# Optimization experiments

Hardware: AMD Instinct MI355X
Metric: run time of the kernel (lower is better)

## Reference

```python
import jax, jax.numpy as jnp
import numpy as np

DIM = 128
D = 2 * DIM           # d_model = dim_hidden * 2
HEADS = 8
DEPTH = 2
DFF = 2048            # PyTorch TransformerEncoderLayer default dim_feedforward
N_NODES = 8192
NO_HOPS = 512
MAX_HOP_LEN = 16
N_LEVELS = 16
MAX_LEV_LEN = NO_HOPS // N_LEVELS  # 32, balanced levels
N_MASKED = 512
N_ENC = 13            # hop tfs 0..3, lev tfs 4..7, graph tfs 8..11, mcm 12 (0,4,8 unused = masked modality)


def setup_inputs() -> dict:
    key = jax.random.key(0)
    ks = jax.random.split(key, 16)
    s = 0.02
    return {
        "tokens": jax.random.normal(ks[0], (4, N_NODES, D), jnp.float32),
        "masked_tokens": jax.random.normal(ks[1], (N_MASKED, D), jnp.float32),
        "hop_nodes": jax.random.normal(ks[2], (1, D), jnp.float32),
        "level_nodes": jax.random.normal(ks[3], (1, D), jnp.float32),
        "graph_nodes": jax.random.normal(ks[4], (1, D), jnp.float32),
        "in_w": jax.random.normal(ks[5], (N_ENC, DEPTH, 3 * D, D), jnp.float32) * s,
        "in_b": jnp.zeros((N_ENC, DEPTH, 3 * D), jnp.float32),
        "out_w": jax.random.normal(ks[6], (N_ENC, DEPTH, D, D), jnp.float32) * s,
        "out_b": jnp.zeros((N_ENC, DEPTH, D), jnp.float32),
        "ff1_w": jax.random.normal(ks[7], (N_ENC, DEPTH, DFF, D), jnp.float32) * s,
        "ff1_b": jnp.zeros((N_ENC, DEPTH, DFF), jnp.float32),
        "ff2_w": jax.random.normal(ks[8], (N_ENC, DEPTH, D, DFF), jnp.float32) * s,
        "ff2_b": jnp.zeros((N_ENC, DEPTH, D), jnp.float32),
        "ln1_w": jnp.ones((N_ENC, DEPTH, D), jnp.float32),
        "ln1_b": jnp.zeros((N_ENC, DEPTH, D), jnp.float32),
        "ln2_w": jnp.ones((N_ENC, DEPTH, D), jnp.float32),
        "ln2_b": jnp.zeros((N_ENC, DEPTH, D), jnp.float32),
        "hop_list": jax.random.randint(ks[9], (3, NO_HOPS, MAX_HOP_LEN), 0, N_NODES),
        "hop_lev": jnp.tile(jnp.arange(NO_HOPS, dtype=jnp.int32) % N_LEVELS, (3, 1)),
        "hop_length": jax.random.randint(ks[10], (3, NO_HOPS), 1, MAX_HOP_LEN + 1),
    }


def _ln(x, w, b):
    mu = jnp.mean(x, axis=-1, keepdims=True)
    var = jnp.mean((x - mu) ** 2, axis=-1, keepdims=True)
    return (x - mu) / jnp.sqrt(var + 1e-5) * w + b


def _layer(x, kpm, p):
    # p: (in_w,in_b,out_w,out_b,ff1_w,ff1_b,ff2_w,ff2_b,ln1_w,ln1_b,ln2_w,ln2_b)
    in_w, in_b, out_w, out_b, f1w, f1b, f2w, f2b, l1w, l1b, l2w, l2b = p
    B, S, Dm = x.shape
    dh = Dm // HEADS
    qkv = x @ in_w.T + in_b                       # [B,S,3D]
    q, k, v = jnp.split(qkv, 3, axis=-1)
    q = q.reshape(B, S, HEADS, dh)
    k = k.reshape(B, S, HEADS, dh)
    v = v.reshape(B, S, HEADS, dh)
    sc = jnp.einsum('bqhd,bkhd->bhqk', q, k) / np.sqrt(dh).astype(np.float32)
    if kpm is not None:
        sc = jnp.where(kpm[:, None, None, :], -1e9, sc)
    a = jax.nn.softmax(sc, axis=-1)
    o = jnp.einsum('bhqk,bkhd->bqhd', a, v).reshape(B, S, Dm) @ out_w.T + out_b
    x = _ln(x + o, l1w, l1b)                      # post-norm (torch default)
    f = jax.nn.relu(x @ f1w.T + f1b) @ f2w.T + f2b
    return _ln(x + f, l2w, l2b)


def _encoder(x, kpm, params, eid):
    for l in range(DEPTH):
        x = _layer(x, kpm, tuple(P[eid, l] for P in params))
    return x


def reference(tokens, masked_tokens, hop_nodes, level_nodes, graph_nodes,
              in_w, in_b, out_w, out_b, ff1_w, ff1_b, ff2_w, ff2_b,
              ln1_w, ln1_b, ln2_w, ln2_b, hop_list, hop_lev, hop_length):
    params = (in_w, in_b, out_w, out_b, ff1_w, ff1_b, ff2_w, ff2_b,
              ln1_w, ln1_b, ln2_w, ln2_b)
    other = []
    for m in range(3):                 # non-masked modalities, modal_k = m+1
        mk = m + 1
        # --- hop transformer: CLS hop token + gathered node tokens per hop ---
        seq = tokens[mk][hop_list[m]]  # [NO_HOPS, L, D]
        seq = jnp.concatenate(
            [jnp.broadcast_to(hop_nodes[None], (NO_HOPS, 1, D)), seq], axis=1)
        kpm = jnp.arange(MAX_HOP_LEN + 1)[None, :] > hop_length[m][:, None]
        hop_tok = _encoder(seq, kpm, params, mk)[:, 0]            # [NO_HOPS, D]
        # --- group hops by level (pack, preserving hop order within level) ---
        lev = hop_lev[m]
        idx = jnp.arange(NO_HOPS)
        pos = jnp.sum((lev[None, :] == lev[:, None]) & (idx[None, :] < idx[:, None]), axis=-1)
        counts = jax.ops.segment_sum(jnp.ones(NO_HOPS, jnp.int32), lev, num_segments=N_LEVELS)
        grid = jnp.zeros((N_LEVELS, MAX_LEV_LEN, D), seq.dtype).at[lev, pos].set(hop_tok)
        grid = jnp.concatenate(
            [jnp.broadcast_to(level_nodes[None], (N_LEVELS, 1, D)), grid], axis=1)
        kpm2 = jnp.arange(MAX_LEV_LEN + 1)[None, :] > counts[:, None]
        lev_tok = _encoder(grid, kpm2, params, 4 + mk)[:, 0]      # [N_LEVELS, D]
        # --- graph transformer over CLS graph token + level tokens ---
        gseq = jnp.concatenate([graph_nodes, lev_tok], axis=0)[None]  # [1, N_LEVELS+1, D]
        g_tok = _encoder(gseq, None, params, 8 + mk)[:, 0]        # [1, D]
        other.append(jnp.concatenate([hop_tok, lev_tok, g_tok], axis=0))
    all_tok = jnp.concatenate([masked_tokens] + other, axis=0)[None]
    pred = _encoder(all_tok, None, params, 12)
    return pred[0, :N_MASKED]
```

## Files before the change

kernel.cpp:

```cpp
#include <hip/hip_runtime.h>

#define D_MODEL 256
#define HEADS 8
#define DH 32
#define DEPTH 2
#define DFF 2048
#define NO_HOPS 512
#define MAX_HOP_LEN 16
#define N_LEVELS 16
#define MAX_LEV_LEN 32
#define N_MASKED 512
#define N_NODES 8192
#define N_FINAL 2099
#define NLAY 26
#define NSPLIT 8

typedef float f32x4 __attribute__((ext_vector_type(4)));
typedef short bf16x8 __attribute__((ext_vector_type(8)));
typedef short short4v __attribute__((ext_vector_type(4)));

#define GLOAD_LDS16(gp, lp) __builtin_amdgcn_global_load_lds( \
    (const __attribute__((address_space(1))) unsigned int*)(gp), \
    (__attribute__((address_space(3))) unsigned int*)(lp), 16, 0, 0)

__device__ __forceinline__ unsigned short f2bf(float f)
{
    unsigned int u = __builtin_bit_cast(unsigned int, f);
    unsigned int r = u + 0x7FFFu + ((u >> 16) & 1u);
    return (unsigned short)(r >> 16);
}

__device__ __forceinline__ float bf2f(unsigned short u)
{
    unsigned int x = (unsigned int)u << 16;
    return __builtin_bit_cast(float, x);
}

__device__ __forceinline__ bf16x8 cvt8(float4 a, float4 b)
{
    bf16x8 r;
    r[0] = (short)f2bf(a.x); r[1] = (short)f2bf(a.y);
    r[2] = (short)f2bf(a.z); r[3] = (short)f2bf(a.w);
    r[4] = (short)f2bf(b.x); r[5] = (short)f2bf(b.y);
    r[6] = (short)f2bf(b.z); r[7] = (short)f2bf(b.w);
    return r;
}

__global__ void cvt_w(const float* __restrict__ src, unsigned short* __restrict__ dst, long n8)
{
    long i = (long)blockIdx.x * blockDim.x + threadIdx.x;
    if (i >= n8) return;
    const float4* s = reinterpret_cast<const float4*>(src) + i * 2;
    float4 a = s[0], b = s[1];
    *reinterpret_cast<bf16x8*>(dst + i * 8) = cvt8(a, b);
}

__global__ __launch_bounds__(256) void gemm_bb64(
    const unsigned short* __restrict__ A, const unsigned short* __restrict__ Wb,
    const float* __restrict__ bias, void* __restrict__ Yv,
    int M, int N, int K, int relu,
    unsigned long rsA, unsigned long xg, unsigned long wg, unsigned long bg, unsigned long yg)
{
    extern __shared__ unsigned short sh[];
    const int grp = blockIdx.z;
    const int t = threadIdx.x;
    const int lane = t & 63, wid = t >> 6;
    const int wr = wid >> 1, wc = wid & 1;
    const int rowbase = blockIdx.y * 64;
    const int colbase = blockIdx.x * 128;
    const unsigned short* Abase = A + (size_t)grp * xg;
    const unsigned short* Wbase = Wb + (size_t)grp * wg;

    const unsigned short* gA[2]; unsigned short* lA[2];
    const unsigned short* gB[4]; unsigned short* lB[4];
    #pragma unroll
    for (int j = 0; j < 2; ++j) {
        int c = j * 256 + t;
        int sr = c >> 3, p = c & 7;
        int lc = p ^ (sr & 7);
        int ar = rowbase + sr; if (ar >= M) ar = M - 1;
        gA[j] = Abase + (size_t)ar * rsA + lc * 8;
        lA[j] = sh + (j * 256 + (t & ~63)) * 8;
    }
    #pragma unroll
    for (int j = 0; j < 4; ++j) {
        int c = j * 256 + t;
        int sr = c >> 3, p = c & 7;
        int lc = p ^ (sr & 7);
        gB[j] = Wbase + (size_t)(colbase + sr) * K + lc * 8;
        lB[j] = sh + 8192 + (j * 256 + (t & ~63)) * 8;
    }

    f32x4 acc[2][4];
    #pragma unroll
    for (int m = 0; m < 2; ++m)
        #pragma unroll
        for (int n = 0; n < 4; ++n)
            acc[m][n] = (f32x4){0.f, 0.f, 0.f, 0.f};

    const int g = lane >> 4, rr = lane & 15;
    const int nt = K >> 6;

    #pragma unroll
    for (int j = 0; j < 2; ++j) GLOAD_LDS16(gA[j], lA[j]);
    #pragma unroll
    for (int j = 0; j < 4; ++j) GLOAD_LDS16(gB[j], lB[j]);

    int buf = 0;
    for (int tt = 0; tt < nt; ++tt) {
        if (tt + 1 < nt) {
            const int k1 = (tt + 1) << 6;
            const int oa = (buf ^ 1) * 4096;
            const int ob = (buf ^ 1) * 8192;
            #pragma unroll
            for (int j = 0; j < 2; ++j) GLOAD_LDS16(gA[j] + k1, lA[j] + oa);
            #pragma unroll
            for (int j = 0; j < 4; ++j) GLOAD_LDS16(gB[j] + k1, lB[j] + ob);
            asm volatile("s_waitcnt vmcnt(6)\n\ts_barrier" ::: "memory");
        } else {
            asm volatile("s_waitcnt vmcnt(0)\n\ts_barrier" ::: "memory");
        }
        const unsigned short* Ab = sh + buf * 4096;
        const unsigned short* Bb = sh + 8192 + buf * 8192;
        #pragma unroll
        for (int ks = 0; ks < 2; ++ks) {
            bf16x8 af[2], bfr[4];
            #pragma unroll
            for (int m = 0; m < 2; ++m) {
                int row = wr * 32 + m * 16 + rr;
                int lc = ks * 4 + g;
                af[m] = *reinterpret_cast<const bf16x8*>(&Ab[row * 64 + ((lc ^ (row & 7)) * 8)]);
            }
            #pragma unroll
            for (int n = 0; n < 4; ++n) {
                int col = wc * 64 + n * 16 + rr;
                int lc = ks * 4 + g;
                bfr[n] = *reinterpret_cast<const bf16x8*>(&Bb[col * 64 + ((lc ^ (col & 7)) * 8)]);
            }
            #pragma unroll
            for (int m = 0; m < 2; ++m)
                #pragma unroll
                for (int n = 0; n < 4; ++n)
                    acc[m][n] = __builtin_amdgcn_mfma_f32_16x16x32_bf16(af[m], bfr[n], acc[m][n], 0, 0, 0);
        }
        asm volatile("s_barrier" ::: "memory");
        buf ^= 1;
    }

    const int rg = lane >> 4;
    const float* bp = bias + (size_t)grp * bg;
    #pragma unroll
    for (int n = 0; n < 4; ++n) {
        int coll = wc * 64 + n * 16 + rr;
        float bv = bp[colbase + coll];
        #pragma unroll
        for (int m = 0; m < 2; ++m) {
            #pragma unroll
            for (int i = 0; i < 4; ++i) {
                int rowl = wr * 32 + m * 16 + rg * 4 + i;
                float v = acc[m][n][i] + bv;
                if (relu) v = fmaxf(v, 0.f);
                sh[rowl * 128 + coll] = f2bf(v);
            }
        }
    }
    __syncthreads();
    unsigned short* Y = (unsigned short*)Yv + (size_t)grp * yg;
    int row = t >> 2, seg = t & 3;
    int grow = rowbase + row;
    if (grow < M) {
        const unsigned short* s = &sh[row * 128 + seg * 32];
        unsigned short* d = Y + (size_t)grow * N + colbase + seg * 32;
        #pragma unroll
        for (int j = 0; j < 4; ++j)
            *reinterpret_cast<bf16x8*>(d + j * 8) = *reinterpret_cast<const bf16x8*>(s + j * 8);
    }
}

__global__ __launch_bounds__(256) void attn_small(
    const unsigned short* __restrict__ QKV, const int* __restrict__ lengths,
    unsigned short* __restrict__ O, int B, int S)
{
    __shared__ __align__(16) unsigned short Ksm[4][32][40];
    __shared__ __align__(16) unsigned short Vsm[4][32][40];
    __shared__ __align__(16) unsigned short Psm[4][32][40];
    const int t = threadIdx.x;
    const int w = t >> 6, lane = t & 63;
    const int l15 = lane & 15, g = lane >> 4;
    int bh = blockIdx.x * 4 + w;
    const int BH = B * HEADS;
    if (bh >= BH) bh = BH - 1;
    const int b = bh >> 3, h = bh & 7;
    const unsigned short* base = QKV + (size_t)b * S * (3 * D_MODEL);
    int len_eff = S - 1;
    if (lengths) { int L = lengths[b]; if (L < len_eff) len_eff = L; }

    {
        int key = lane >> 1, hf = lane & 1;
        int kg = key < S ? key : S - 1;
        const unsigned short* kp = base + (size_t)kg * (3 * D_MODEL) + D_MODEL + h * DH + hf * 16;
        bf16x8 k0 = *reinterpret_cast<const bf16x8*>(kp);
        bf16x8 k1 = *reinterpret_cast<const bf16x8*>(kp + 8);
        *reinterpret_cast<bf16x8*>(&Ksm[w][key][hf * 16]) = k0;
        *reinterpret_cast<bf16x8*>(&Ksm[w][key][hf * 16 + 8]) = k1;
        const unsigned short* vp = kp + D_MODEL;
        bf16x8 v0 = *reinterpret_cast<const bf16x8*>(vp);
        bf16x8 v1 = *reinterpret_cast<const bf16x8*>(vp + 8);
        #pragma unroll
        for (int i = 0; i < 8; ++i) {
            Vsm[w][hf * 16 + i][key]     = (unsigned short)v0[i];
            Vsm[w][hf * 16 + 8 + i][key] = (unsigned short)v1[i];
        }
    }
    bf16x8 qa[2];
    #pragma unroll
    for (int qf = 0; qf < 2; ++qf) {
        int q = qf * 16 + l15; if (q > S - 1) q = S - 1;
        qa[qf] = *reinterpret_cast<const bf16x8*>(base + (size_t)q * (3 * D_MODEL) + h * DH + g * 8);
    }
    __syncthreads();

    const float scale = 0.17677669529663687f;
    const f32x4 zero = (f32x4){0.f,0.f,0.f,0.f};
    f32x4 sc[2][2];
    #pragma unroll
    for (int kf = 0; kf < 2; ++kf) {
        bf16x8 kb = *reinterpret_cast<const bf16x8*>(&Ksm[w][kf * 16 + l15][g * 8]);
        #pragma unroll
        for (int qf = 0; qf < 2; ++qf)
            sc[qf][kf] = __builtin_amdgcn_mfma_f32_16x16x32_bf16(qa[qf], kb, zero, 0, 0, 0);
    }
    float rsum[2][4];
    #pragma unroll
    for (int qf = 0; qf < 2; ++qf) {
        #pragma unroll
        for (int kf = 0; kf < 2; ++kf) {
            if (kf * 16 + l15 > len_eff) sc[qf][kf] = (f32x4){-1e9f,-1e9f,-1e9f,-1e9f};
            else sc[qf][kf] *= scale;
        }
        #pragma unroll
        for (int r = 0; r < 4; ++r) {
            float mx = fmaxf(sc[qf][0][r], sc[qf][1][r]);
            mx = fmaxf(mx, __shfl_xor(mx, 1, 64));
            mx = fmaxf(mx, __shfl_xor(mx, 2, 64));
            mx = fmaxf(mx, __shfl_xor(mx, 4, 64));
            mx = fmaxf(mx, __shfl_xor(mx, 8, 64));
            float s0 = __expf(sc[qf][0][r] - mx);
            float s1 = __expf(sc[qf][1][r] - mx);
            sc[qf][0][r] = s0;
            sc[qf][1][r] = s1;
            float ss = s0 + s1;
            ss += __shfl_xor(ss, 1, 64);
            ss += __shfl_xor(ss, 2, 64);
            ss += __shfl_xor(ss, 4, 64);
            ss += __shfl_xor(ss, 8, 64);
            rsum[qf][r] = ss;
        }
    }
    #pragma unroll
    for (int qf = 0; qf < 2; ++qf)
        #pragma unroll
        for (int kf = 0; kf < 2; ++kf)
            #pragma unroll
            for (int r = 0; r < 4; ++r)
                Psm[w][qf * 16 + g * 4 + r][kf * 16 + l15] = f2bf(sc[qf][kf][r]);
    __syncthreads();

    f32x4 o[2][2];
    #pragma unroll
    for (int df = 0; df < 2; ++df) {
        bf16x8 vb = *reinterpret_cast<const bf16x8*>(&Vsm[w][df * 16 + l15][g * 8]);
        #pragma unroll
        for (int qf = 0; qf < 2; ++qf) {
            bf16x8 pa = *reinterpret_cast<const bf16x8*>(&Psm[w][qf * 16 + l15][g * 8]);
            o[qf][df] = __builtin_amdgcn_mfma_f32_16x16x32_bf16(pa, vb, zero, 0, 0, 0);
        }
    }
    #pragma unroll
    for (int qf = 0; qf < 2; ++qf)
        #pragma unroll
        for (int r = 0; r < 4; ++r) {
            int q = qf * 16 + g * 4 + r;
            if (q < S) {
                float inv = 1.f / rsum[qf][r];
                #pragma unroll
                for (int df = 0; df < 2; ++df)
                    O[((size_t)b * S + q) * D_MODEL + h * DH + df * 16 + l15] = f2bf(o[qf][df][r] * inv);
            }
        }
}

template<int SPLIT>
__global__ __launch_bounds__(256) void attn_flash(
    const unsigned short* __restrict__ QKV, const int* __restrict__ lengths,
    unsigned short* __restrict__ O, int B, int S,
    int NSv, float* __restrict__ pAcc, float* __restrict__ pMS)
{
    __shared__ __align__(16) unsigned short Kt[64][32];
    __shared__ __align__(16) unsigned short Vt[32][64];
    __shared__ __align__(16) unsigned short Pw[4][16][64];

    const int t = threadIdx.x;
    const int lane = t & 63, wid = t >> 6;
    const int l15 = lane & 15, g = lane >> 4;
    const int b = SPLIT ? 0 : blockIdx.z;
    const int sp = SPLIT ? blockIdx.z : 0;
    const int h = blockIdx.y;
    const int qb = blockIdx.x * 64 + wid * 16;
    const unsigned short* base = QKV + (size_t)b * S * (3 * D_MODEL);

    int len_eff = S - 1;
    if (lengths) { int L = lengths[b]; if (L < len_eff) len_eff = L; }

    const float scale = 0.17677669529663687f;
    int qrow = qb + l15; if (qrow > S - 1) qrow = S - 1;
    bf16x8 qa = *reinterpret_cast<const bf16x8*>(base + (size_t)qrow * (3 * D_MODEL) + h * DH + g * 8);

    float m[4], sum[4];
    f32x4 o[2];
    #pragma unroll
    for (int r = 0; r < 4; ++r) { m[r] = -3.0e38f; sum[r] = 0.f; }
    o[0] = (f32x4){0.f,0.f,0.f,0.f};
    o[1] = (f32x4){0.f,0.f,0.f,0.f};

    const int kl = t >> 2, cg = t & 3;
    const int ntiles_all = (S + 63) >> 6;
    int tstart = 0, tend = ntiles_all;
    if (SPLIT) {
        int chunkT = (ntiles_all + NSv - 1) / NSv;
        tstart = sp * chunkT;
        tend = tstart + chunkT;
        if (tend > ntiles_all) tend = ntiles_all;
    }

    for (int tt = tstart; tt < tend; ++tt) {
        const int kbase = tt * 64;
        {
            int key = kbase + kl; if (key > S - 1) key = S - 1;
            const unsigned short* kp = base + (size_t)key * (3 * D_MODEL) + D_MODEL + h * DH + cg * 8;
            *reinterpret_cast<bf16x8*>(&Kt[kl][cg * 8]) = *reinterpret_cast<const bf16x8*>(kp);
            bf16x8 vv = *reinterpret_cast<const bf16x8*>(kp + D_MODEL);
            #pragma unroll
            for (int i = 0; i < 8; ++i) {
                int d = cg * 8 + i;
                int c = ((kl >> 3) ^ (d & 7)) * 8 + (kl & 7);
                Vt[d][c] = (unsigned short)vv[i];
            }
        }
        __syncthreads();

        f32x4 sc[4];
        const f32x4 zero = (f32x4){0.f,0.f,0.f,0.f};
        #pragma unroll
        for (int f = 0; f < 4; ++f) {
            bf16x8 kf = *reinterpret_cast<const bf16x8*>(&Kt[f * 16 + l15][g * 8]);
            sc[f] = __builtin_amdgcn_mfma_f32_16x16x32_bf16(qa, kf, zero, 0, 0, 0);
            sc[f] *= scale;
        }
        #pragma unroll
        for (int f = 0; f < 4; ++f) {
            if (kbase + f * 16 + l15 > len_eff)
                sc[f] = (f32x4){-1e9f,-1e9f,-1e9f,-1e9f};
        }
        float cr[4];
        #pragma unroll
        for (int r = 0; r < 4; ++r) {
            float mx = fmaxf(fmaxf(sc[0][r], sc[1][r]), fmaxf(sc[2][r], sc[3][r]));
            mx = fmaxf(mx, __shfl_xor(mx, 1, 64));
            mx = fmaxf(mx, __shfl_xor(mx, 2, 64));
            mx = fmaxf(mx, __shfl_xor(mx, 4, 64));
            mx = fmaxf(mx, __shfl_xor(mx, 8, 64));
            float nm = fmaxf(m[r], mx);
            cr[r] = __expf(m[r] - nm);
            m[r] = nm;
            float ssum = 0.f;
            #pragma unroll
            for (int f = 0; f < 4; ++f) {
                float e = __expf(sc[f][r] - nm);
                sc[f][r] = e;
                ssum += e;
            }
            ssum += __shfl_xor(ssum, 1, 64);
            ssum += __shfl_xor(ssum, 2, 64);
            ssum += __shfl_xor(ssum, 4, 64);
            ssum += __shfl_xor(ssum, 8, 64);
            sum[r] = sum[r] * cr[r] + ssum;
            o[0][r] *= cr[r];
            o[1][r] *= cr[r];
        }
        #pragma unroll
        for (int f = 0; f < 4; ++f) {
            int chunk = f * 2 + (l15 >> 3);
            #pragma unroll
            for (int r = 0; r < 4; ++r) {
                int row = g * 4 + r;
                Pw[wid][row][(chunk ^ (row & 7)) * 8 + (l15 & 7)] = f2bf(sc[f][r]);
            }
        }
        #pragma unroll
        for (int s = 0; s < 2; ++s) {
            bf16x8 pa = *reinterpret_cast<const bf16x8*>(
                &Pw[wid][l15][((s * 4 + g) ^ (l15 & 7)) * 8]);
            #pragma unroll
            for (int jf = 0; jf < 2; ++jf) {
                int d = jf * 16 + l15;
                bf16x8 vb = *reinterpret_cast<const bf16x8*>(
                    &Vt[d][((s * 4 + g) ^ (d & 7)) * 8]);
                o[jf] = __builtin_amdgcn_mfma_f32_16x16x32_bf16(pa, vb, o[jf], 0, 0, 0);
            }
        }
        __syncthreads();
    }

    if (SPLIT) {
        #pragma unroll
        for (int r = 0; r < 4; ++r) {
            int qout = qb + g * 4 + r;
            if (qout < S) {
                size_t pb = ((size_t)qout * HEADS + h) * NSv + sp;
                pAcc[pb * 32 + l15]      = o[0][r];
                pAcc[pb * 32 + 16 + l15] = o[1][r];
                if (l15 == 0) { pMS[pb * 2] = m[r]; pMS[pb * 2 + 1] = sum[r]; }
            }
        }
    } else {
        #pragma unroll
        for (int r = 0; r < 4; ++r) {
            float inv = 1.f / sum[r];
            int qout = qb + g * 4 + r;
            if (qout < S) {
                #pragma unroll
                for (int jf = 0; jf < 2; ++jf)
                    O[((size_t)b * S + qout) * D_MODEL + h * DH + jf * 16 + l15] = f2bf(o[jf][r] * inv);
            }
        }
    }
}

__global__ void attn_merge(const float* __restrict__ pAcc, const float* __restrict__ pMS,
                           unsigned short* __restrict__ O, int S, int NS)
{
    int idx = blockIdx.x * blockDim.x + threadIdx.x;
    if (idx >= S * HEADS * DH) return;
    int d = idx & 31;
    int h = (idx >> 5) & 7;
    int q = idx >> 8;
    size_t base = ((size_t)q * HEADS + h) * NS;
    float mstar = -3.0e38f;
    for (int s = 0; s < NS; ++s) mstar = fmaxf(mstar, pMS[(base + s) * 2]);
    float ssum = 0.f, acc = 0.f;
    for (int s = 0; s < NS; ++s) {
        float mi = pMS[(base + s) * 2];
        float si = pMS[(base + s) * 2 + 1];
        float w = __expf(mi - mstar);
        ssum += si * w;
        acc += pAcc[(base + s) * 32 + d] * w;
    }
    O[(size_t)q * D_MODEL + h * DH + d] = f2bf(acc / ssum);
}

__global__ void add_ln_g(const unsigned short* __restrict__ Xin, const unsigned short* __restrict__ R,
                         const float* __restrict__ w, const float* __restrict__ b,
                         unsigned short* __restrict__ Xout,
                         int M, int rows_pg, unsigned long wg, unsigned long rsX)
{
    int row = blockIdx.x * 4 + (threadIdx.x >> 6);
    int lane = threadIdx.x & 63;
    if (row >= M) return;
    int g = row / rows_pg;
    const float* wp = w + (size_t)g * wg;
    const float* bp = b + (size_t)g * wg;
    short4v xv = *reinterpret_cast<const short4v*>(Xin + (size_t)row * rsX + lane * 4);
    short4v rv = *reinterpret_cast<const short4v*>(R + (size_t)row * D_MODEL + lane * 4);
    float v[4];
    float sum = 0.f;
    #pragma unroll
    for (int j = 0; j < 4; ++j) {
        v[j] = bf2f((unsigned short)xv[j]) + bf2f((unsigned short)rv[j]);
        sum += v[j];
    }
    #pragma unroll
    for (int o = 32; o > 0; o >>= 1) sum += __shfl_xor(sum, o, 64);
    float mu = sum * (1.f / D_MODEL);
    float sq = 0.f;
    #pragma unroll
    for (int j = 0; j < 4; ++j) { float dd = v[j] - mu; sq += dd * dd; }
    #pragma unroll
    for (int o = 32; o > 0; o >>= 1) sq += __shfl_xor(sq, o, 64);
    float inv = rsqrtf(sq * (1.f / D_MODEL) + 1e-5f);
    short4v xb;
    #pragma unroll
    for (int j = 0; j < 4; ++j) {
        float out = (v[j] - mu) * inv * wp[lane * 4 + j] + bp[lane * 4 + j];
        xb[j] = (short)f2bf(out);
    }
    *reinterpret_cast<short4v*>(Xout + (size_t)row * D_MODEL + lane * 4) = xb;
}

__global__ void build_hop_seq_g(const float* __restrict__ tok, const int* __restrict__ hlist,
                                const float* __restrict__ hop_nodes,
                                unsigned short* __restrict__ Xb, int nm)
{
    int idx = blockIdx.x * blockDim.x + threadIdx.x;
    const int per = NO_HOPS * (MAX_HOP_LEN + 1) * D_MODEL;
    if (idx >= nm * per) return;
    int g = idx / per, r = idx % per;
    int d = r & 255;
    int rest = r >> 8;
    int p = rest % (MAX_HOP_LEN + 1);
    int hh = rest / (MAX_HOP_LEN + 1);
    float v;
    if (p == 0) v = hop_nodes[d];
    else {
        int node = hlist[(size_t)g * NO_HOPS * MAX_HOP_LEN + hh * MAX_HOP_LEN + p - 1];
        v = tok[(size_t)g * N_NODES * D_MODEL + (size_t)node * D_MODEL + d];
    }
    Xb[idx] = f2bf(v);
}

__global__ void compute_pos_g(const int* __restrict__ hop_lev, int* __restrict__ pos,
                              int* __restrict__ counts)
{
    int g = blockIdx.x;
    const int* lev = hop_lev + (size_t)g * NO_HOPS;
    int i = threadIdx.x;
    int li = lev[i];
    int p = 0;
    for (int j = 0; j < i; ++j) p += (lev[j] == li);
    pos[(size_t)g * NO_HOPS + i] = p;
    if (i < N_LEVELS) {
        int c = 0;
        for (int j = 0; j < NO_HOPS; ++j) c += (lev[j] == i);
        counts[(size_t)g * N_LEVELS + i] = c;
    }
}

__global__ void build_level_init_g(const float* __restrict__ level_nodes,
                                   unsigned short* __restrict__ Gb, int nm)
{
    int idx = blockIdx.x * blockDim.x + threadIdx.x;
    const int per = N_LEVELS * (MAX_LEV_LEN + 1) * D_MODEL;
    if (idx >= nm * per) return;
    int r = idx % per;
    int d = r & 255;
    int p = (r >> 8) % (MAX_LEV_LEN + 1);
    float v = (p == 0) ? level_nodes[d] : 0.f;
    Gb[idx] = f2bf(v);
}

__global__ void scatter_hops_g(const float* __restrict__ hop_tok, const int* __restrict__ hop_lev,
                               const int* __restrict__ pos,
                               unsigned short* __restrict__ Gb, int nm)
{
    int idx = blockIdx.x * blockDim.x + threadIdx.x;
    const int per = NO_HOPS * D_MODEL;
    if (idx >= nm * per) return;
    int g = idx / per, r = idx % per;
    int d = r & 255;
    int i = r >> 8;
    int lv = hop_lev[(size_t)g * NO_HOPS + i];
    int ps = pos[(size_t)g * NO_HOPS + i];
    size_t dst = (size_t)g * N_LEVELS * (MAX_LEV_LEN + 1) * D_MODEL +
                 ((size_t)lv * (MAX_LEV_LEN + 1) + 1 + ps) * D_MODEL + d;
    Gb[dst] = f2bf(hop_tok[idx]);
}

__global__ void build_graph_seq_g(const float* __restrict__ graph_nodes,
                                  const float* __restrict__ lev_tok,
                                  unsigned short* __restrict__ Xb, int nm)
{
    int idx = blockIdx.x * blockDim.x + threadIdx.x;
    const int per = (N_LEVELS + 1) * D_MODEL;
    if (idx >= nm * per) return;
    int g = idx / per, r = idx % per;
    int d = r & 255;
    int p = r >> 8;
    float v = (p == 0) ? graph_nodes[d]
                       : lev_tok[(size_t)g * N_LEVELS * D_MODEL + (size_t)(p - 1) * D_MODEL + d];
    Xb[idx] = f2bf(v);
}

__global__ void build_final_seq(const float* __restrict__ masked, const float* __restrict__ hoptok,
                                const float* __restrict__ levtok, const float* __restrict__ gtok,
                                unsigned short* __restrict__ Xb)
{
    int idx = blockIdx.x * blockDim.x + threadIdx.x;
    const int total = N_FINAL * D_MODEL;
    if (idx >= total) return;
    int d = idx & 255;
    int r = idx >> 8;
    float v;
    if (r < N_MASKED) v = masked[idx];
    else {
        int t = r - N_MASKED;
        int m = t / 529;
        int w = t % 529;
        if (w < 512)      v = hoptok[((size_t)m * 512 + w) * D_MODEL + d];
        else if (w < 528) v = levtok[((size_t)m * 16 + (w - 512)) * D_MODEL + d];
        else              v = gtok[m * D_MODEL + d];
    }
    Xb[idx] = f2bf(v);
}

__global__ void extract_cls(const unsigned short* __restrict__ Xb, float* __restrict__ out,
                            int B, int S)
{
    int idx = blockIdx.x * blockDim.x + threadIdx.x;
    if (idx >= B * D_MODEL) return;
    int b = idx >> 8;
    int d = idx & 255;
    out[idx] = bf2f(Xb[(size_t)b * S * D_MODEL + d]);
}

__global__ void copy_out_kernel(const unsigned short* __restrict__ src, float* __restrict__ dst, int n)
{
    int i = blockIdx.x * blockDim.x + threadIdx.x;
    if (i < n) dst[i] = bf2f(src[i]);
}

struct WB {
    const unsigned short *inw, *outw, *f1w, *f2w;
    const float *in_b, *out_b, *ff1_b, *ff2_b, *ln1_w, *ln1_b, *ln2_w, *ln2_b;
};

#define SZ_INW  ((size_t)3 * D_MODEL * D_MODEL)
#define SZ_OUTW ((size_t)D_MODEL * D_MODEL)
#define SZ_F1W  ((size_t)DFF * D_MODEL)
#define SZ_F2W  ((size_t)D_MODEL * DFF)
#define GS_INW  ((unsigned long)DEPTH * SZ_INW)
#define GS_INB  ((unsigned long)DEPTH * 3 * D_MODEL)
#define GS_OUTW ((unsigned long)DEPTH * SZ_OUTW)
#define GS_OUTB ((unsigned long)DEPTH * D_MODEL)
#define GS_F1W  ((unsigned long)DEPTH * SZ_F1W)
#define GS_F1B  ((unsigned long)DEPTH * DFF)
#define GS_F2W  ((unsigned long)DEPTH * SZ_F2W)
#define GS_F2B  ((unsigned long)DEPTH * D_MODEL)
#define GS_LN   ((unsigned long)DEPTH * D_MODEL)

static void launch_gemm(const unsigned short* A, unsigned long rsA, const unsigned short* Wb,
                        const float* bias, void* Yv, int M, int N, int K, int relu, int nm,
                        unsigned long xg, unsigned long wg, unsigned long bg, unsigned long yg,
                        hipStream_t stream)
{
    dim3 grid(N / 128, (M + 63) / 64, nm);
    hipLaunchKernelGGL(gemm_bb64, grid, dim3(256), 49152, stream,
                       A, Wb, bias, Yv, M, N, K, relu, rsA, xg, wg, bg, yg);
}

static void run_layer_g(unsigned short* Xb, unsigned short* QKV, unsigned short* O,
                        unsigned short* Tb, unsigned short* FF,
                        unsigned short* XC1, unsigned short* TC, unsigned short* XC2,
                        float* skAcc, float* skMS,
                        int ff_rows, int nm, int Btot, int S,
                        const int* lengths, const WB& W, int eid0, int l, int last,
                        hipStream_t stream)
{
    const int Bpg = Btot / nm;
    const int Mpg = Bpg * S;
    const size_t il = (size_t)eid0 * DEPTH + l;
    launch_gemm(Xb, D_MODEL, W.inw + il * SZ_INW, W.in_b + il * 3 * D_MODEL, QKV,
                Mpg, 3 * D_MODEL, D_MODEL, 0, nm,
                (unsigned long)Mpg * D_MODEL, GS_INW, GS_INB, (unsigned long)Mpg * 3 * D_MODEL,
                stream);
    {
        int qspan = S;
        if (last && Btot == 1 && S >= 1024) qspan = N_MASKED;
        int qtiles = (qspan + 63) / 64;
        if (S <= 32) {
            int blocks = (Btot * HEADS + 3) / 4;
            hipLaunchKernelGGL(attn_small, dim3(blocks), dim3(256), 0, stream,
                               QKV, lengths, O, Btot, S);
        } else if (Btot == 1 && S >= 1024) {
            dim3 grid(qtiles, HEADS, NSPLIT);
            hipLaunchKernelGGL((attn_flash<1>), grid, dim3(256), 0, stream,
                               QKV, lengths, O, Btot, S, NSPLIT, skAcc, skMS);
            int tot = qspan * HEADS * DH;
            hipLaunchKernelGGL(attn_merge, dim3((tot + 255) / 256), dim3(256), 0, stream,
                               skAcc, skMS, O, qspan, NSPLIT);
        } else {
            dim3 grid(qtiles, HEADS, Btot);
            hipLaunchKernelGGL((attn_flash<0>), grid, dim3(256), 0, stream,
                               QKV, lengths, O, Btot, S, 1, (float*)nullptr, (float*)nullptr);
        }
    }
    if (!last) {
        launch_gemm(O, D_MODEL, W.outw + il * SZ_OUTW, W.out_b + il * D_MODEL, Tb,
                    Mpg, D_MODEL, D_MODEL, 0, nm,
                    (unsigned long)Mpg * D_MODEL, GS_OUTW, GS_OUTB, (unsigned long)Mpg * D_MODEL,
                    stream);
        int Mtot = nm * Mpg;
        hipLaunchKernelGGL(add_ln_g, dim3((Mtot + 3) / 4), dim3(256), 0, stream,
                           Xb, Tb, W.ln1_w + il * D_MODEL, W.ln1_b + il * D_MODEL, Xb,
                           Mtot, Mpg, GS_LN, (unsigned long)D_MODEL);
        for (int m0 = 0; m0 < Mpg; m0 += ff_rows) {
            int mc = (Mpg - m0 < ff_rows) ? (Mpg - m0) : ff_rows;
            launch_gemm(Xb + (size_t)m0 * D_MODEL, D_MODEL,
                        W.f1w + il * SZ_F1W, W.ff1_b + il * DFF, FF,
                        mc, DFF, D_MODEL, 1, nm,
                        (unsigned long)Mpg * D_MODEL, GS_F1W, GS_F1B, (unsigned long)mc * DFF,
                        stream);
            launch_gemm(FF, DFF, W.f2w + il * SZ_F2W, W.ff2_b + il * D_MODEL,
                        Tb + (size_t)m0 * D_MODEL,
                        mc, D_MODEL, DFF, 0, nm,
                        (unsigned long)mc * DFF, GS_F2W, GS_F2B, (unsigned long)Mpg * D_MODEL,
                        stream);
        }
        hipLaunchKernelGGL(add_ln_g, dim3((Mtot + 3) / 4), dim3(256), 0, stream,
                           Xb, Tb, W.ln2_w + il * D_MODEL, W.ln2_b + il * D_MODEL, Xb,
                           Mtot, Mpg, GS_LN, (unsigned long)D_MODEL);
    } else {
        int Mc; unsigned long rsC;
        if (S >= 1024) { Mc = N_MASKED; rsC = (unsigned long)D_MODEL; }
        else           { Mc = Bpg;      rsC = (unsigned long)S * D_MODEL; }
        int Mtc = nm * Mc;
        launch_gemm(O, rsC, W.outw + il * SZ_OUTW, W.out_b + il * D_MODEL, TC,
                    Mc, D_MODEL, D_MODEL, 0, nm,
                    (unsigned long)Mpg * D_MODEL, GS_OUTW, GS_OUTB, (unsigned long)Mc * D_MODEL,
                    stream);
        hipLaunchKernelGGL(add_ln_g, dim3((Mtc + 3) / 4), dim3(256), 0, stream,
                           Xb, TC, W.ln1_w + il * D_MODEL, W.ln1_b + il * D_MODEL, XC1,
                           Mtc, Mc, GS_LN, rsC);
        launch_gemm(XC1, D_MODEL, W.f1w + il * SZ_F1W, W.ff1_b + il * DFF, FF,
                    Mc, DFF, D_MODEL, 1, nm,
                    (unsigned long)Mc * D_MODEL, GS_F1W, GS_F1B, (unsigned long)Mc * DFF,
                    stream);
        launch_gemm(FF, DFF, W.f2w + il * SZ_F2W, W.ff2_b + il * D_MODEL, TC,
                    Mc, D_MODEL, DFF, 0, nm,
                    (unsigned long)Mc * DFF, GS_F2W, GS_F2B, (unsigned long)Mc * D_MODEL,
                    stream);
        hipLaunchKernelGGL(add_ln_g, dim3((Mtc + 3) / 4), dim3(256), 0, stream,
                           XC1, TC, W.ln2_w + il * D_MODEL, W.ln2_b + il * D_MODEL, XC2,
                           Mtc, Mc, GS_LN, (unsigned long)D_MODEL);
    }
}

static void run_encoder_g(unsigned short* Xb, unsigned short* QKV, unsigned short* O,
                          unsigned short* Tb, unsigned short* FF,
                          unsigned short* XC1, unsigned short* TC, unsigned short* XC2,
                          float* skAcc, float* skMS,
                          int ff_rows, int nm, int Btot, int S,
                          const int* lengths, const WB& W, int eid0, hipStream_t stream)
{
    for (int l = 0; l < DEPTH; ++l)
        run_layer_g(Xb, QKV, O, Tb, FF, XC1, TC, XC2, skAcc, skMS, ff_rows, nm, Btot, S,
                    lengths, W, eid0, l, l == DEPTH - 1, stream);
}

extern "C" void kernel_launch(void* const* d_in, const int* in_sizes, int n_in,
                              void* d_out, int out_size, void* d_ws, size_t ws_size,
                              hipStream_t stream)
{
    const float* tokens        = (const float*)d_in[0];
    const float* masked_tokens = (const float*)d_in[1];
    const float* hop_nodes     = (const float*)d_in[2];
    const float* level_nodes   = (const float*)d_in[3];
    const float* graph_nodes   = (const float*)d_in[4];
    const float* in_w  = (const float*)d_in[5];
    const float* in_b  = (const float*)d_in[6];
    const float* out_w = (const float*)d_in[7];
    const float* out_b = (const float*)d_in[8];
    const float* ff1_w = (const float*)d_in[9];
    const float* ff1_b = (const float*)d_in[10];
    const float* ff2_w = (const float*)d_in[11];
    const float* ff2_b = (const float*)d_in[12];
    const float* ln1_w = (const float*)d_in[13];
    const float* ln1_b = (const float*)d_in[14];
    const float* ln2_w = (const float*)d_in[15];
    const float* ln2_b = (const float*)d_in[16];
    const int* hop_list   = (const int*)d_in[17];
    const int* hop_lev    = (const int*)d_in[18];
    const int* hop_length = (const int*)d_in[19];

    float* ws = (float*)d_ws;
    size_t cap = ws_size / sizeof(float);
    const size_t MH = (size_t)NO_HOPS * (MAX_HOP_LEN + 1) * D_MODEL;

    const size_t N_INW  = (size_t)NLAY * SZ_INW;
    const size_t N_OUTW = (size_t)NLAY * SZ_OUTW;
    const size_t N_F1W  = (size_t)NLAY * SZ_F1W;
    const size_t N_F2W  = (size_t)NLAY * SZ_F2W;
    const size_t WBF = (N_INW + N_OUTW + N_F1W + N_F2W) / 2;
    const size_t SK_ACC = (size_t)NSPLIT * N_FINAL * HEADS * DH;
    const size_t SK_MS  = (size_t)NSPLIT * N_FINAL * HEADS * 2;
    const size_t SZC = (size_t)3 * N_MASKED * D_MODEL / 2;

    int NM = 3;
    {
        size_t fixed3 = 3 * MH / 2 + 3 * MH * 3 / 2 + 3 * MH / 2 + 3 * MH / 2
                      + (size_t)3 * NO_HOPS * D_MODEL + 3 * N_LEVELS * D_MODEL + 768 + 4096
                      + WBF + SK_ACC + SK_MS + 3 * SZC;
        size_t ffmin = (size_t)3 * 128 * DFF / 2;
        if (fixed3 + ffmin > cap) NM = 1;
    }

    size_t off = 0;
    auto take = [&](size_t n) { float* p = ws + off; off += (n + 7) & ~(size_t)7; return p; };
    size_t xsz = (size_t)NM * MH;
    unsigned short* Xb     = (unsigned short*)take(xsz / 2);
    unsigned short* QKV    = (unsigned short*)take(xsz * 3 / 2);
    unsigned short* O      = (unsigned short*)take(xsz / 2);
    unsigned short* Tb     = (unsigned short*)take(xsz / 2);
    float*          HOPTOK = take((size_t)3 * NO_HOPS * D_MODEL);
    float*          LEVTOK = take((size_t)3 * N_LEVELS * D_MODEL);
    float*          GTOK   = take((size_t)3 * D_MODEL);
    int*            POS    = (int*)take(2048);
    int*            COUNTS = POS + 3 * NO_HOPS;
    float*          SKACC  = take(SK_ACC);
    float*          SKMS   = take(SK_MS);
    unsigned short* XC1    = (unsigned short*)take(SZC);
    unsigned short* TC     = (unsigned short*)take(SZC);
    unsigned short* XC2    = (unsigned short*)take(SZC);
    unsigned short* WINW   = (unsigned short*)take(N_INW / 2);
    unsigned short* WOUTW  = (unsigned short*)take(N_OUTW / 2);
    unsigned short* WF1    = (unsigned short*)take(N_F1W / 2);
    unsigned short* WF2    = (unsigned short*)take(N_F2W / 2);
    unsigned short* FF     = (unsigned short*)(ws + off);
    size_t ff_ushorts = (cap > off) ? (cap - off) * 2 : 0;
    int ff_rows = (int)(ff_ushorts / ((size_t)NM * DFF));
    int max_rows = NO_HOPS * (MAX_HOP_LEN + 1);
    if (ff_rows > max_rows) ff_rows = max_rows;
    if (ff_rows > 2048) ff_rows &= ~127;
    if (ff_rows < 128) ff_rows = 128;

    hipLaunchKernelGGL(cvt_w, dim3((N_INW / 8 + 255) / 256), dim3(256), 0, stream, in_w,  WINW,  N_INW / 8);
    hipLaunchKernelGGL(cvt_w, dim3((N_OUTW / 8 + 255) / 256), dim3(256), 0, stream, out_w, WOUTW, N_OUTW / 8);
    hipLaunchKernelGGL(cvt_w, dim3((N_F1W / 8 + 255) / 256), dim3(256), 0, stream, ff1_w, WF1,   N_F1W / 8);
    hipLaunchKernelGGL(cvt_w, dim3((N_F2W / 8 + 255) / 256), dim3(256), 0, stream, ff2_w, WF2,   N_F2W / 8);

    WB W;
    W.inw = WINW; W.outw = WOUTW; W.f1w = WF1; W.f2w = WF2;
    W.in_b = in_b; W.out_b = out_b; W.ff1_b = ff1_b; W.ff2_b = ff2_b;
    W.ln1_w = ln1_w; W.ln1_b = ln1_b; W.ln2_w = ln2_w; W.ln2_b = ln2_b;

    for (int ms = 0; ms < 3; ms += NM) {
        const int nm = NM;
        {
            int total = nm * NO_HOPS * (MAX_HOP_LEN + 1) * D_MODEL;
            hipLaunchKernelGGL(build_hop_seq_g, dim3((total + 255) / 256), dim3(256), 0, stream,
                               tokens + (size_t)(ms + 1) * N_NODES * D_MODEL,
                               hop_list + (size_t)ms * NO_HOPS * MAX_HOP_LEN,
                               hop_nodes, Xb, nm);
        }
        run_encoder_g(Xb, QKV, O, Tb, FF, XC1, TC, XC2, SKACC, SKMS, ff_rows,
                      nm, nm * NO_HOPS, MAX_HOP_LEN + 1,
                      hop_length + (size_t)ms * NO_HOPS, W, 1 + ms, stream);
        {
            int B = nm * NO_HOPS;
            hipLaunchKernelGGL(extract_cls, dim3((B * D_MODEL + 255) / 256), dim3(256), 0, stream,
                               XC2, HOPTOK + (size_t)ms * NO_HOPS * D_MODEL, B, 1);
        }

        hipLaunchKernelGGL(compute_pos_g, dim3(nm), dim3(NO_HOPS), 0, stream,
                           hop_lev + (size_t)ms * NO_HOPS, POS, COUNTS);
        {
            int total = nm * N_LEVELS * (MAX_LEV_LEN + 1) * D_MODEL;
            hipLaunchKernelGGL(build_level_init_g, dim3((total + 255) / 256), dim3(256), 0, stream,
                               level_nodes, Xb, nm);
        }
        {
            int total = nm * NO_HOPS * D_MODEL;
            hipLaunchKernelGGL(scatter_hops_g, dim3((total + 255) / 256), dim3(256), 0, stream,
                               HOPTOK + (size_t)ms * NO_HOPS * D_MODEL,
                               hop_lev + (size_t)ms * NO_HOPS, POS, Xb, nm);
        }
        run_encoder_g(Xb, QKV, O, Tb, FF, XC1, TC, XC2, SKACC, SKMS, ff_rows,
                      nm, nm * N_LEVELS, MAX_LEV_LEN + 1,
                      COUNTS, W, 5 + ms, stream);
        {
            int B = nm * N_LEVELS;
            hipLaunchKernelGGL(extract_cls, dim3((B * D_MODEL + 255) / 256), dim3(256), 0, stream,
                               XC2, LEVTOK + (size_t)ms * N_LEVELS * D_MODEL, B, 1);
        }

        {
            int total = nm * (N_LEVELS + 1) * D_MODEL;
            hipLaunchKernelGGL(build_graph_seq_g, dim3((total + 255) / 256), dim3(256), 0, stream,
                               graph_nodes, LEVTOK + (size_t)ms * N_LEVELS * D_MODEL, Xb, nm);
        }
        run_encoder_g(Xb, QKV, O, Tb, FF, XC1, TC, XC2, SKACC, SKMS, ff_rows,
                      nm, nm, N_LEVELS + 1,
                      nullptr, W, 9 + ms, stream);
        {
            int B = nm;
            hipLaunchKernelGGL(extract_cls, dim3((B * D_MODEL + 255) / 256), dim3(256), 0, stream,
                               XC2, GTOK + (size_t)ms * D_MODEL, B, 1);
        }
    }

    {
        int total = N_FINAL * D_MODEL;
        hipLaunchKernelGGL(build_final_seq, dim3((total + 255) / 256), dim3(256), 0, stream,
                           masked_tokens, HOPTOK, LEVTOK, GTOK, Xb);
    }
    run_encoder_g(Xb, QKV, O, Tb, FF, XC1, TC, XC2, SKACC, SKMS, ff_rows,
                  1, 1, N_FINAL, nullptr, W, 12, stream);

    {
        int n = N_MASKED * D_MODEL;
        hipLaunchKernelGGL(copy_out_kernel, dim3((n + 255) / 256), dim3(256), 0, stream,
                           XC2, (float*)d_out, n);
    }
}
```

Baseline: 698.6 us.

## Fuse residual add and LayerNorm into full-width N=256 GEMM epilogue

Adds a GEMM kernel whose 64-row tile covers all 256 output columns, so the residual add and LayerNorm run in the epilogue from shared memory. It replaces the separate out-proj/FF2 GEMMs and the add_ln_g launches, removing the intermediate write and re-read and several kernel launches. In exchange the full-width tile gives fewer blocks per GEMM, which lowers parallelism on small M, and each block does a long K=2048 loop for FF2.

```diff
diff --git a/kernel.cpp b/kernel.cpp
--- a/kernel.cpp
+++ b/kernel.cpp
@@ -174,6 +174,163 @@
         #pragma unroll
         for (int j = 0; j < 4; ++j)
             *reinterpret_cast<bf16x8*>(d + j * 8) = *reinterpret_cast<const bf16x8*>(s + j * 8);
+    }
+}
+
+__global__ __launch_bounds__(256) void gemm_n256_ln(
+    const unsigned short* __restrict__ A, const unsigned short* __restrict__ R,
+    const unsigned short* __restrict__ Wb, const float* __restrict__ bias,
+    const float* __restrict__ lnw, const float* __restrict__ lnb,
+    unsigned short* __restrict__ Y,
+    int M, int K,
+    unsigned long rsA, unsigned long rsR,
+    unsigned long xg, unsigned long rg_, unsigned long wg, unsigned long bg,
+    unsigned long lg, unsigned long yg)
+{
+    extern __shared__ unsigned short sh[];
+    const int grp = blockIdx.z;
+    const int t = threadIdx.x;
+    const int lane = t & 63, wid = t >> 6;
+    const int rowbase = blockIdx.x * 64;
+    const unsigned short* Abase = A + (size_t)grp * xg;
+    const unsigned short* Rg = R + (size_t)grp * rg_;
+    const unsigned short* Wbase = Wb + (size_t)grp * wg;
+
+    const unsigned short* gA; unsigned short* lA;
+    {
+        int sr = t >> 2, p = t & 3;
+        int lc = p ^ (sr & 3);
+        int ar = rowbase + sr; if (ar >= M) ar = M - 1;
+        gA = Abase + (size_t)ar * rsA + lc * 8;
+        lA = sh + (t & ~63) * 8;
+    }
+    const unsigned short* gB[4]; unsigned short* lB[4];
+    #pragma unroll
+    for (int j = 0; j < 4; ++j) {
+        int c = j * 256 + t;
+        int sr = c >> 2, p = c & 3;
+        int lc = p ^ (sr & 3);
+        gB[j] = Wbase + (size_t)sr * K + lc * 8;
+        lB[j] = sh + 4096 + (j * 256 + (t & ~63)) * 8;
+    }
+
+    f32x4 acc[4][4];
+    #pragma unroll
+    for (int m = 0; m < 4; ++m)
+        #pragma unroll
+        for (int n = 0; n < 4; ++n)
+            acc[m][n] = (f32x4){0.f, 0.f, 0.f, 0.f};
+
+    const int g = lane >> 4, rr = lane & 15;
+    const int nt = K >> 5;
+
+    GLOAD_LDS16(gA, lA);
+    #pragma unroll
+    for (int j = 0; j < 4; ++j) GLOAD_LDS16(gB[j], lB[j]);
+
+    int buf = 0;
+    for (int tt = 0; tt < nt; ++tt) {
+        if (tt + 1 < nt) {
+            const int k1 = (tt + 1) << 5;
+            GLOAD_LDS16(gA + k1, lA + (buf ^ 1) * 2048);
+            #pragma unroll
+            for (int j = 0; j < 4; ++j) GLOAD_LDS16(gB[j] + k1, lB[j] + (buf ^ 1) * 8192);
+            asm volatile("s_waitcnt vmcnt(5)\n\ts_barrier" ::: "memory");
+        } else {
+            asm volatile("s_waitcnt vmcnt(0)\n\ts_barrier" ::: "memory");
+        }
+        const unsigned short* Ab = sh + buf * 2048;
+        const unsigned short* Bb = sh + 4096 + buf * 8192;
+        bf16x8 af[4], bfr[4];
+        #pragma unroll
+        for (int m = 0; m < 4; ++m) {
+            int row = m * 16 + rr;
+            af[m] = *reinterpret_cast<const bf16x8*>(&Ab[row * 32 + ((g ^ (row & 3)) * 8)]);
+        }
+        #pragma unroll
+        for (int n = 0; n < 4; ++n) {
+            int col = wid * 64 + n * 16 + rr;
+            bfr[n] = *reinterpret_cast<const bf16x8*>(&Bb[col * 32 + ((g ^ (col & 3)) * 8)]);
+        }
+        #pragma unroll
+        for (int m = 0; m < 4; ++m)
+            #pragma unroll
+            for (int n = 0; n < 4; ++n)
+                acc[m][n] = __builtin_amdgcn_mfma_f32_16x16x32_bf16(af[m], bfr[n], acc[m][n], 0, 0, 0);
+        asm volatile("s_barrier" ::: "memory");
+        buf ^= 1;
+    }
+
+    const int PD = 264;
+    unsigned short* shOut = sh + 4096;
+    const float* bp = bias + (size_t)grp * bg;
+    #pragma unroll
+    for (int n = 0; n < 4; ++n) {
+        int coll = wid * 64 + n * 16 + rr;
+        float bv = bp[coll];
+        #pragma unroll
+        for (int m = 0; m < 4; ++m) {
+            #pragma unroll
+            for (int i = 0; i < 4; ++i) {
+                int rowl = m * 16 + g * 4 + i;
+                shOut[rowl * PD + coll] = f2bf(acc[m][n][i] + bv);
+            }
+        }
+    }
+    __syncthreads();
+
+    {
+        int row = t >> 2, seg = t & 3;
+        int grow = rowbase + row;
+        int valid = grow < M;
+        int gr = valid ? grow : M - 1;
+        const unsigned short* rp = Rg + (size_t)gr * rsR + seg * 64;
+        const unsigned short* xp = &shOut[row * PD + seg * 64];
+        float sum = 0.f;
+        #pragma unroll
+        for (int j = 0; j < 8; ++j) {
+            bf16x8 xv = *reinterpret_cast<const bf16x8*>(xp + j * 8);
+            bf16x8 rv = *reinterpret_cast<const bf16x8*>(rp + j * 8);
+            #pragma unroll
+            for (int k = 0; k < 8; ++k)
+                sum += bf2f((unsigned short)xv[k]) + bf2f((unsigned short)rv[k]);
+        }
+        sum += __shfl_xor(sum, 1, 64);
+        sum += __shfl_xor(sum, 2, 64);
+        float mu = sum * (1.f / D_MODEL);
+        float sq = 0.f;
+        #pragma unroll
+        for (int j = 0; j < 8; ++j) {
+            bf16x8 xv = *reinterpret_cast<const bf16x8*>(xp + j * 8);
+            bf16x8 rv = *reinterpret_cast<const bf16x8*>(rp + j * 8);
+            #pragma unroll
+            for (int k = 0; k < 8; ++k) {
+                float v = bf2f((unsigned short)xv[k]) + bf2f((unsigned short)rv[k]);
+                float d = v - mu;
+                sq += d * d;
+            }
+        }
+        sq += __shfl_xor(sq, 1, 64);
+        sq += __shfl_xor(sq, 2, 64);
+        float inv = rsqrtf(sq * (1.f / D_MODEL) + 1e-5f);
+        const float* wlp = lnw + (size_t)grp * lg + seg * 64;
+        const float* blp = lnb + (size_t)grp * lg + seg * 64;
+        unsigned short* yo = Y + (size_t)grp * yg + (size_t)gr * D_MODEL + seg * 64;
+        if (valid) {
+            #pragma unroll
+            for (int j = 0; j < 8; ++j) {
+                bf16x8 xv = *reinterpret_cast<const bf16x8*>(xp + j * 8);
+                bf16x8 rv = *reinterpret_cast<const bf16x8*>(rp + j * 8);
+                bf16x8 ov;
+                #pragma unroll
+                for (int k = 0; k < 8; ++k) {
+                    float v = bf2f((unsigned short)xv[k]) + bf2f((unsigned short)rv[k]);
+                    float out = (v - mu) * inv * wlp[j * 8 + k] + blp[j * 8 + k];
+                    ov[k] = (short)f2bf(out);
+                }
+                *reinterpret_cast<bf16x8*>(yo + j * 8) = ov;
+            }
+        }
     }
 }
 
@@ -459,44 +616,6 @@
     O[(size_t)q * D_MODEL + h * DH + d] = f2bf(acc / ssum);
 }
 
-__global__ void add_ln_g(const unsigned short* __restrict__ Xin, const unsigned short* __restrict__ R,
-                         const float* __restrict__ w, const float* __restrict__ b,
-                         unsigned short* __restrict__ Xout,
-                         int M, int rows_pg, unsigned long wg, unsigned long rsX)
-{
-    int row = blockIdx.x * 4 + (threadIdx.x >> 6);
-    int lane = threadIdx.x & 63;
-    if (row >= M) return;
-    int g = row / rows_pg;
-    const float* wp = w + (size_t)g * wg;
-    const float* bp = b + (size_t)g * wg;
-    short4v xv = *reinterpret_cast<const short4v*>(Xin + (size_t)row * rsX + lane * 4);
-    short4v rv = *reinterpret_cast<const short4v*>(R + (size_t)row * D_MODEL + lane * 4);
-    float v[4];
-    float sum = 0.f;
-    #pragma unroll
-    for (int j = 0; j < 4; ++j) {
-        v[j] = bf2f((unsigned short)xv[j]) + bf2f((unsigned short)rv[j]);
-        sum += v[j];
-    }
-    #pragma unroll
-    for (int o = 32; o > 0; o >>= 1) sum += __shfl_xor(sum, o, 64);
-    float mu = sum * (1.f / D_MODEL);
-    float sq = 0.f;
-    #pragma unroll
-    for (int j = 0; j < 4; ++j) { float dd = v[j] - mu; sq += dd * dd; }
-    #pragma unroll
-    for (int o = 32; o > 0; o >>= 1) sq += __shfl_xor(sq, o, 64);
-    float inv = rsqrtf(sq * (1.f / D_MODEL) + 1e-5f);
-    short4v xb;
-    #pragma unroll
-    for (int j = 0; j < 4; ++j) {
-        float out = (v[j] - mu) * inv * wp[lane * 4 + j] + bp[lane * 4 + j];
-        xb[j] = (short)f2bf(out);
-    }
-    *reinterpret_cast<short4v*>(Xout + (size_t)row * D_MODEL + lane * 4) = xb;
-}
-
 __global__ void build_hop_seq_g(const float* __restrict__ tok, const int* __restrict__ hlist,
                                 const float* __restrict__ hop_nodes,
                                 unsigned short* __restrict__ Xb, int nm)
@@ -647,6 +766,20 @@
                        A, Wb, bias, Yv, M, N, K, relu, rsA, xg, wg, bg, yg);
 }
 
+static void launch_gemm_ln(const unsigned short* A, unsigned long rsA, unsigned long xg,
+                           const unsigned short* R, unsigned long rsR, unsigned long rg,
+                           const unsigned short* Wb, unsigned long wg,
+                           const float* bias, unsigned long bg,
+                           const float* lnw, const float* lnb, unsigned long lg,
+                           unsigned short* Y, unsigned long yg,
+                           int M, int K, int nm, hipStream_t stream)
+{
+    dim3 grid((M + 63) / 64, 1, nm);
+    hipLaunchKernelGGL(gemm_n256_ln, grid, dim3(256), 41984, stream,
+                       A, R, Wb, bias, lnw, lnb, Y, M, K,
+                       rsA, rsR, xg, rg, wg, bg, lg, yg);
+}
+
 static void run_layer_g(unsigned short* Xb, unsigned short* QKV, unsigned short* O,
                         unsigned short* Tb, unsigned short* FF,
                         unsigned short* XC1, unsigned short* TC, unsigned short* XC2,
@@ -655,6 +788,7 @@
                         const int* lengths, const WB& W, int eid0, int l, int last,
                         hipStream_t stream)
 {
+    (void)Tb; (void)TC;
     const int Bpg = Btot / nm;
     const int Mpg = Bpg * S;
     const size_t il = (size_t)eid0 * DEPTH + l;
@@ -684,14 +818,13 @@
         }
     }
     if (!last) {
-        launch_gemm(O, D_MODEL, W.outw + il * SZ_OUTW, W.out_b + il * D_MODEL, Tb,
-                    Mpg, D_MODEL, D_MODEL, 0, nm,
-                    (unsigned long)Mpg * D_MODEL, GS_OUTW, GS_OUTB, (unsigned long)Mpg * D_MODEL,
-                    stream);
-        int Mtot = nm * Mpg;
-        hipLaunchKernelGGL(add_ln_g, dim3((Mtot + 3) / 4), dim3(256), 0, stream,
-                           Xb, Tb, W.ln1_w + il * D_MODEL, W.ln1_b + il * D_MODEL, Xb,
-                           Mtot, Mpg, GS_LN, (unsigned long)D_MODEL);
+        launch_gemm_ln(O, D_MODEL, (unsigned long)Mpg * D_MODEL,
+                       Xb, D_MODEL, (unsigned long)Mpg * D_MODEL,
+                       W.outw + il * SZ_OUTW, GS_OUTW,
+                       W.out_b + il * D_MODEL, GS_OUTB,
+                       W.ln1_w + il * D_MODEL, W.ln1_b + il * D_MODEL, GS_LN,
+                       Xb, (unsigned long)Mpg * D_MODEL,
+                       Mpg, D_MODEL, nm, stream);
         for (int m0 = 0; m0 < Mpg; m0 += ff_rows) {
             int mc = (Mpg - m0 < ff_rows) ? (Mpg - m0) : ff_rows;
             launch_gemm(Xb + (size_t)m0 * D_MODEL, D_MODEL,
@@ -699,38 +832,36 @@
                         mc, DFF, D_MODEL, 1, nm,
                         (unsigned long)Mpg * D_MODEL, GS_F1W, GS_F1B, (unsigned long)mc * DFF,
                         stream);
-            launch_gemm(FF, DFF, W.f2w + il * SZ_F2W, W.ff2_b + il * D_MODEL,
-                        Tb + (size_t)m0 * D_MODEL,
-                        mc, D_MODEL, DFF, 0, nm,
-                        (unsigned long)mc * DFF, GS_F2W, GS_F2B, (unsigned long)Mpg * D_MODEL,
-                        stream);
-        }
-        hipLaunchKernelGGL(add_ln_g, dim3((Mtot + 3) / 4), dim3(256), 0, stream,
-                           Xb, Tb, W.ln2_w + il * D_MODEL, W.ln2_b + il * D_MODEL, Xb,
-                           Mtot, Mpg, GS_LN, (unsigned long)D_MODEL);
+            launch_gemm_ln(FF, DFF, (unsigned long)mc * DFF,
+                           Xb + (size_t)m0 * D_MODEL, D_MODEL, (unsigned long)Mpg * D_MODEL,
+                           W.f2w + il * SZ_F2W, GS_F2W,
+                           W.ff2_b + il * D_MODEL, GS_F2B,
+                           W.ln2_w + il * D_MODEL, W.ln2_b + il * D_MODEL, GS_LN,
+                           Xb + (size_t)m0 * D_MODEL, (unsigned long)Mpg * D_MODEL,
+                           mc, DFF, nm, stream);
+        }
     } else {
         int Mc; unsigned long rsC;
         if (S >= 1024) { Mc = N_MASKED; rsC = (unsigned long)D_MODEL; }
         else           { Mc = Bpg;      rsC = (unsigned long)S * D_MODEL; }
-        int Mtc = nm * Mc;
-        launch_gemm(O, rsC, W.outw + il * SZ_OUTW, W.out_b + il * D_MODEL, TC,
-                    Mc, D_MODEL, D_MODEL, 0, nm,
-                    (unsigned long)Mpg * D_MODEL, GS_OUTW, GS_OUTB, (unsigned long)Mc * D_MODEL,
-                    stream);
-        hipLaunchKernelGGL(add_ln_g, dim3((Mtc + 3) / 4), dim3(256), 0, stream,
-                           Xb, TC, W.ln1_w + il * D_MODEL, W.ln1_b + il * D_MODEL, XC1,
-                           Mtc, Mc, GS_LN, rsC);
+        launch_gemm_ln(O, rsC, (unsigned long)Mpg * D_MODEL,
+                       Xb, rsC, (unsigned long)Mpg * D_MODEL,
+                       W.outw + il * SZ_OUTW, GS_OUTW,
+                       W.out_b + il * D_MODEL, GS_OUTB,
+                       W.ln1_w + il * D_MODEL, W.ln1_b + il * D_MODEL, GS_LN,
+                       XC1, (unsigned long)Mc * D_MODEL,
+                       Mc, D_MODEL, nm, stream);
         launch_gemm(XC1, D_MODEL, W.f1w + il * SZ_F1W, W.ff1_b + il * DFF, FF,
                     Mc, DFF, D_MODEL, 1, nm,
                     (unsigned long)Mc * D_MODEL, GS_F1W, GS_F1B, (unsigned long)Mc * DFF,
                     stream);
-        launch_gemm(FF, DFF, W.f2w + il * SZ_F2W, W.ff2_b + il * D_MODEL, TC,
-                    Mc, D_MODEL, DFF, 0, nm,
-                    (unsigned long)Mc * DFF, GS_F2W, GS_F2B, (unsigned long)Mc * D_MODEL,
-                    stream);
-        hipLaunchKernelGGL(add_ln_g, dim3((Mtc + 3) / 4), dim3(256), 0, stream,
-                           XC1, TC, W.ln2_w + il * D_MODEL, W.ln2_b + il * D_MODEL, XC2,
-                           Mtc, Mc, GS_LN, (unsigned long)D_MODEL);
+        launch_gemm_ln(FF, DFF, (unsigned long)Mc * DFF,
+                       XC1, D_MODEL, (unsigned long)Mc * D_MODEL,
+                       W.f2w + il * SZ_F2W, GS_F2W,
+                       W.ff2_b + il * D_MODEL, GS_F2B,
+                       W.ln2_w + il * D_MODEL, W.ln2_b + il * D_MODEL, GS_LN,
+                       XC2, (unsigned long)Mc * D_MODEL,
+                       Mc, DFF, nm, stream);
     }
 }
 
```

After: 890.7 us. +27.5%, slower.
